# Optimization experiments

Measured on AMD Instinct MI355X. Metric: run time of the kernel, lower is better.

Reference implementation:

```python
import jax, jax.numpy as jnp
import numpy as np

BN_EPS = 1e-5
TAU = 1.0  # gumbel temperature

def setup_inputs() -> dict:
    key = jax.random.key(0)
    ks = jax.random.split(key, 6)
    B, O, F, H, HID = 32, 4096, 256, 8, 128
    x = jax.random.normal(ks[0], (B, O, F), dtype=jnp.float32)
    gumbel_noise = jax.random.gumbel(ks[1], (B, O, H), dtype=jnp.float32)
    W_in = jax.random.normal(ks[2], (F, HID), dtype=jnp.float32) * (1.0 / np.sqrt(F))
    b_in = jnp.zeros((HID,), jnp.float32)
    W_blk = jax.random.normal(ks[3], (HID, HID), dtype=jnp.float32) * (1.0 / np.sqrt(HID))
    b_blk = jnp.zeros((HID,), jnp.float32)
    bn_gamma = jnp.ones((HID,), jnp.float32)
    bn_beta = jnp.zeros((HID,), jnp.float32)
    W_fc = jax.random.normal(ks[4], (HID, H), dtype=jnp.float32) * (1.0 / np.sqrt(HID))
    b_fc = jnp.zeros((H,), jnp.float32)
    return {"x": x, "gumbel_noise": gumbel_noise, "W_in": W_in, "b_in": b_in,
            "W_blk": W_blk, "b_blk": b_blk, "bn_gamma": bn_gamma, "bn_beta": bn_beta,
            "W_fc": W_fc, "b_fc": b_fc}

def reference(x, gumbel_noise, W_in, b_in, W_blk, b_blk, bn_gamma, bn_beta, W_fc, b_fc):
    B, O, F = x.shape
    xf = x.reshape(B * O, F)
    # DynamicNetwork head: input linear + relu, one residual block (Linear+BN+ReLU), fc
    h = jax.nn.relu(xf @ W_in + b_in)  # (B*O, HID)
    z = h @ W_blk + b_blk
    mu = z.mean(axis=0)
    var = z.var(axis=0)  # biased var, matches BatchNorm training normalization
    z = (z - mu) * jax.lax.rsqrt(var + BN_EPS) * bn_gamma + bn_beta
    h = jax.nn.relu(z) + h  # residual
    logits = (h @ W_fc + b_fc).reshape(B, O, -1)  # (B, O, H)
    # mask out zero-norm observations
    mask = (jnp.linalg.norm(x, axis=2) != 0)[..., None].astype(x.dtype)  # (B, O, 1)
    logits = logits * mask
    # gumbel softmax over observation dim (soft)
    w = jax.nn.softmax((logits + gumbel_noise) / TAU, axis=1)  # (B, O, H)
    # weighted sum pooling: algebraically the repeat-multiply-sum in the original
    pooled = jnp.einsum('boh,bof->bhf', w, x)  # (B, H, F)
    return pooled.reshape(B, -1)  # (B, H*F)
```

## Files before the change

kernel.cpp:

```cpp
#include <hip/hip_runtime.h>
#include <hip/hip_bf16.h>
#include <math.h>

#define MB_ 131072
#define F_  256
#define HID_ 128
#define H_  8
#define O_  4096
#define B_  32

typedef __attribute__((ext_vector_type(8))) short short8;
typedef __attribute__((ext_vector_type(4))) float f32x4;

static __device__ __forceinline__ unsigned short f2bf(float f) {
    unsigned int u = __float_as_uint(f);
    unsigned int r = (u + 0x7fffu + ((u >> 16) & 1u)) >> 16;
    return (unsigned short)r;
}
static __device__ __forceinline__ float bf2f(unsigned short u) {
    return __uint_as_float(((unsigned int)u) << 16);
}

__global__ __launch_bounds__(256) void k_prep(
    const float* __restrict__ W_in, const float* __restrict__ W_blk,
    unsigned short* __restrict__ WinT, unsigned short* __restrict__ WblkT)
{
    const int idx = blockIdx.x * 256 + threadIdx.x;
    if (idx < 32768) {
        const int n = idx >> 8, k = idx & 255;
        WinT[idx] = f2bf(W_in[(size_t)k * HID_ + n]);
    } else {
        const int i2 = idx - 32768;
        const int n = i2 >> 7, k = i2 & 127;
        WblkT[i2] = f2bf(W_blk[(size_t)k * HID_ + n]);
    }
}

__global__ __launch_bounds__(256) void k_phaseA(
    const float* __restrict__ x, const unsigned short* __restrict__ WinT,
    const unsigned short* __restrict__ WblkT,
    const float* __restrict__ b_in, const float* __restrict__ b_blk,
    unsigned short* __restrict__ h_out, float* __restrict__ mask_out,
    float* __restrict__ sumP, float* __restrict__ sumsqP)
{
    __shared__ unsigned short a_s[128 * 40];
    __shared__ unsigned short b_s[128 * 40];
    __shared__ unsigned short hb_s[128 * 136];
    __shared__ float msum_s[128];
    __shared__ float csum_s[128], csumsq_s[128];

    const int tid = threadIdx.x;
    const int R0 = blockIdx.x * 128;
    const int lp_r = tid >> 3;
    const int lp_c = tid & 7;
    const int wave = tid >> 6;
    const int wrow = wave >> 1, wcol = wave & 1;
    const int lane = tid & 63;
    const int lm = lane & 15, quad = lane >> 4;

    if (tid < 128) { msum_s[tid] = 0.f; csum_s[tid] = 0.f; csumsq_s[tid] = 0.f; }
    float ms[4] = {0.f, 0.f, 0.f, 0.f};

    f32x4 acc[4][4];
#pragma unroll
    for (int i = 0; i < 4; i++)
#pragma unroll
        for (int j = 0; j < 4; j++) acc[i][j] = (f32x4){0.f, 0.f, 0.f, 0.f};

    for (int kt = 0; kt < 8; kt++) {
#pragma unroll
        for (int p = 0; p < 4; p++) {
            const int r = lp_r + 32 * p;
            const float4 v = *(const float4*)(x + (size_t)(R0 + r) * F_ + kt * 32 + lp_c * 4);
            ms[p] += v.x * v.x + v.y * v.y + v.z * v.z + v.w * v.w;
            ushort4 o;
            o.x = f2bf(v.x); o.y = f2bf(v.y); o.z = f2bf(v.z); o.w = f2bf(v.w);
            *(ushort4*)(&a_s[r * 40 + lp_c * 4]) = o;
        }
#pragma unroll
        for (int p = 0; p < 4; p++) {
            const int n = lp_r + 32 * p;
            const ushort4 wv = *(const ushort4*)(WinT + (size_t)n * F_ + kt * 32 + lp_c * 4);
            *(ushort4*)(&b_s[n * 40 + lp_c * 4]) = wv;
        }
        __syncthreads();
        short8 af[4], bfr[4];
#pragma unroll
        for (int mi = 0; mi < 4; mi++)
            af[mi] = *(const short8*)(&a_s[(wrow * 64 + mi * 16 + lm) * 40 + quad * 8]);
#pragma unroll
        for (int ni = 0; ni < 4; ni++)
            bfr[ni] = *(const short8*)(&b_s[(wcol * 64 + ni * 16 + lm) * 40 + quad * 8]);
#pragma unroll
        for (int mi = 0; mi < 4; mi++)
#pragma unroll
            for (int ni = 0; ni < 4; ni++)
                acc[mi][ni] = __builtin_amdgcn_mfma_f32_16x16x32_bf16(af[mi], bfr[ni], acc[mi][ni], 0, 0, 0);
        __syncthreads();
    }

#pragma unroll
    for (int p = 0; p < 4; p++) atomicAdd(&msum_s[lp_r + 32 * p], ms[p]);
    {
        float bcol[4];
#pragma unroll
        for (int ni = 0; ni < 4; ni++) bcol[ni] = b_in[wcol * 64 + ni * 16 + lm];
#pragma unroll
        for (int mi = 0; mi < 4; mi++)
#pragma unroll
            for (int r = 0; r < 4; r++) {
                const int row = wrow * 64 + mi * 16 + quad * 4 + r;
#pragma unroll
                for (int ni = 0; ni < 4; ni++) {
                    const int col = wcol * 64 + ni * 16 + lm;
                    hb_s[row * 136 + col] = f2bf(fmaxf(acc[mi][ni][r] + bcol[ni], 0.f));
                }
            }
    }
    __syncthreads();

    {
        const int row = tid >> 1, half = tid & 1;
#pragma unroll
        for (int c8 = 0; c8 < 8; c8++) {
            const short8 v = *(const short8*)(&hb_s[row * 136 + half * 64 + c8 * 8]);
            *(short8*)(h_out + (size_t)(R0 + row) * HID_ + half * 64 + c8 * 8) = v;
        }
    }
    if (tid < 128) mask_out[R0 + tid] = (msum_s[tid] != 0.f) ? 1.f : 0.f;

#pragma unroll
    for (int i = 0; i < 4; i++)
#pragma unroll
        for (int j = 0; j < 4; j++) acc[i][j] = (f32x4){0.f, 0.f, 0.f, 0.f};
    for (int kt = 0; kt < 4; kt++) {
#pragma unroll
        for (int p = 0; p < 4; p++) {
            const int n = lp_r + 32 * p;
            const ushort4 wv = *(const ushort4*)(WblkT + (size_t)n * HID_ + kt * 32 + lp_c * 4);
            *(ushort4*)(&b_s[n * 40 + lp_c * 4]) = wv;
        }
        __syncthreads();
        short8 af[4], bfr[4];
#pragma unroll
        for (int mi = 0; mi < 4; mi++)
            af[mi] = *(const short8*)(&hb_s[(wrow * 64 + mi * 16 + lm) * 136 + kt * 32 + quad * 8]);
#pragma unroll
        for (int ni = 0; ni < 4; ni++)
            bfr[ni] = *(const short8*)(&b_s[(wcol * 64 + ni * 16 + lm) * 40 + quad * 8]);
#pragma unroll
        for (int mi = 0; mi < 4; mi++)
#pragma unroll
            for (int ni = 0; ni < 4; ni++)
                acc[mi][ni] = __builtin_amdgcn_mfma_f32_16x16x32_bf16(af[mi], bfr[ni], acc[mi][ni], 0, 0, 0);
        __syncthreads();
    }

    {
        float bcol[4];
#pragma unroll
        for (int ni = 0; ni < 4; ni++) bcol[ni] = b_blk[wcol * 64 + ni * 16 + lm];
        float s_c[4] = {0.f, 0.f, 0.f, 0.f}, ss_c[4] = {0.f, 0.f, 0.f, 0.f};
#pragma unroll
        for (int mi = 0; mi < 4; mi++)
#pragma unroll
            for (int r = 0; r < 4; r++)
#pragma unroll
                for (int ni = 0; ni < 4; ni++) {
                    const float zv = acc[mi][ni][r] + bcol[ni];
                    s_c[ni] += zv;
                    ss_c[ni] += zv * zv;
                }
#pragma unroll
        for (int ni = 0; ni < 4; ni++) {
            atomicAdd(&csum_s[wcol * 64 + ni * 16 + lm], s_c[ni]);
            atomicAdd(&csumsq_s[wcol * 64 + ni * 16 + lm], ss_c[ni]);
        }
    }
    __syncthreads();
    if (tid < 128) {
        sumP[(size_t)blockIdx.x * 128 + tid] = csum_s[tid];
        sumsqP[(size_t)blockIdx.x * 128 + tid] = csumsq_s[tid];
    }
}

__global__ __launch_bounds__(256) void k_bnfin(
    const float* __restrict__ sumP, const float* __restrict__ sumsqP,
    const float* __restrict__ gamma, const float* __restrict__ beta,
    float* __restrict__ scale, float* __restrict__ shift)
{
    const int c = blockIdx.x;
    const int tid = threadIdx.x;
    float s = 0.f, ss = 0.f;
    for (int i = tid; i < 1024; i += 256) {
        s  += sumP[(size_t)i * 128 + c];
        ss += sumsqP[(size_t)i * 128 + c];
    }
#pragma unroll
    for (int off = 32; off; off >>= 1) {
        s  += __shfl_xor(s, off, 64);
        ss += __shfl_xor(ss, off, 64);
    }
    __shared__ float rs[4], rss[4];
    const int wid = tid >> 6, lane = tid & 63;
    if (lane == 0) { rs[wid] = s; rss[wid] = ss; }
    __syncthreads();
    if (tid == 0) {
        const float S  = rs[0] + rs[1] + rs[2] + rs[3];
        const float SS = rss[0] + rss[1] + rss[2] + rss[3];
        const float inv_m = 1.0f / (float)MB_;
        const float mu = S * inv_m;
        const float var = SS * inv_m - mu * mu;
        const float sc = gamma[c] * rsqrtf(var + 1e-5f);
        scale[c] = sc;
        shift[c] = beta[c] - mu * sc;
    }
}

__global__ __launch_bounds__(256) void k_phaseC(
    const unsigned short* __restrict__ h_in, const unsigned short* __restrict__ WblkT,
    const float* __restrict__ b_blk,
    const float* __restrict__ scale, const float* __restrict__ shift,
    const float* __restrict__ W_fc, const float* __restrict__ b_fc,
    const float* __restrict__ mask, const float* __restrict__ gumbel,
    float* __restrict__ t_bho)
{
    __shared__ unsigned short hb_s[128 * 136];
    __shared__ unsigned short b_s[128 * 40];
    __shared__ float wfc_s[128 * 8];
    __shared__ float sc_s[128], sh_s[128];

    const int tid = threadIdx.x;
    const int R0 = blockIdx.x * 128;
    const int wave = tid >> 6;
    const int wrow = wave >> 1, wcol = wave & 1;
    const int lane = tid & 63;
    const int lm = lane & 15, quad = lane >> 4;
    const int lp_r = tid >> 3, lp_c = tid & 7;

    for (int i = tid; i < 1024; i += 256) wfc_s[i] = W_fc[i];
    if (tid < 128) { sc_s[tid] = scale[tid]; sh_s[tid] = shift[tid]; }
    {
        const int row = tid >> 1, half = tid & 1;
#pragma unroll
        for (int c8 = 0; c8 < 8; c8++) {
            const short8 v = *(const short8*)(h_in + (size_t)(R0 + row) * HID_ + half * 64 + c8 * 8);
            *(short8*)(&hb_s[row * 136 + half * 64 + c8 * 8]) = v;
        }
    }
    __syncthreads();

    f32x4 acc[4][4];
#pragma unroll
    for (int i = 0; i < 4; i++)
#pragma unroll
        for (int j = 0; j < 4; j++) acc[i][j] = (f32x4){0.f, 0.f, 0.f, 0.f};
    for (int kt = 0; kt < 4; kt++) {
#pragma unroll
        for (int p = 0; p < 4; p++) {
            const int n = lp_r + 32 * p;
            const ushort4 wv = *(const ushort4*)(WblkT + (size_t)n * HID_ + kt * 32 + lp_c * 4);
            *(ushort4*)(&b_s[n * 40 + lp_c * 4]) = wv;
        }
        __syncthreads();
        short8 af[4], bfr[4];
#pragma unroll
        for (int mi = 0; mi < 4; mi++)
            af[mi] = *(const short8*)(&hb_s[(wrow * 64 + mi * 16 + lm) * 136 + kt * 32 + quad * 8]);
#pragma unroll
        for (int ni = 0; ni < 4; ni++)
            bfr[ni] = *(const short8*)(&b_s[(wcol * 64 + ni * 16 + lm) * 40 + quad * 8]);
#pragma unroll
        for (int mi = 0; mi < 4; mi++)
#pragma unroll
            for (int ni = 0; ni < 4; ni++)
                acc[mi][ni] = __builtin_amdgcn_mfma_f32_16x16x32_bf16(af[mi], bfr[ni], acc[mi][ni], 0, 0, 0);
        __syncthreads();
    }

    {
        float bcol[4];
#pragma unroll
        for (int ni = 0; ni < 4; ni++) bcol[ni] = b_blk[wcol * 64 + ni * 16 + lm];
#pragma unroll
        for (int mi = 0; mi < 4; mi++)
#pragma unroll
            for (int r = 0; r < 4; r++) {
                const int row = wrow * 64 + mi * 16 + quad * 4 + r;
#pragma unroll
                for (int ni = 0; ni < 4; ni++) {
                    const int col = wcol * 64 + ni * 16 + lm;
                    const float zv = acc[mi][ni][r] + bcol[ni];
                    const float hv = bf2f(hb_s[row * 136 + col]);
                    const float hb = fmaxf(zv * sc_s[col] + sh_s[col], 0.f) + hv;
                    hb_s[row * 136 + col] = f2bf(hb);
                }
            }
    }
    __syncthreads();

    if (tid < 128) {
        const int row = tid;
        const int grow = R0 + row;
        const int b = grow >> 12, o = grow & 4095;
        float a8[8];
#pragma unroll
        for (int j = 0; j < 8; j++) a8[j] = 0.f;
#pragma unroll 4
        for (int k8 = 0; k8 < 16; k8++) {
            const short8 hv8 = *(const short8*)(&hb_s[row * 136 + k8 * 8]);
#pragma unroll
            for (int e = 0; e < 8; e++) {
                const float hv = bf2f((unsigned short)hv8[e]);
                const int k = k8 * 8 + e;
#pragma unroll
                for (int j = 0; j < 8; j++) a8[j] += hv * wfc_s[k * 8 + j];
            }
        }
        const float mk = mask[grow];
        const float* gp = gumbel + (size_t)grow * 8;
#pragma unroll
        for (int j = 0; j < 8; j++) {
            const float t = (a8[j] + b_fc[j]) * mk + gp[j];
            t_bho[((size_t)(b * 8 + j)) * O_ + o] = t;
        }
    }
}

__global__ __launch_bounds__(256) void k_softmax(
    const float* __restrict__ t_in, float* __restrict__ w_out)
{
    const int bh = blockIdx.x;
    const int tid = threadIdx.x;
    const float* tp = t_in + (size_t)bh * O_;
    float4 v[4];
    float mx = -3.4e38f;
#pragma unroll
    for (int it = 0; it < 4; it++) {
        v[it] = *(const float4*)(tp + it * 1024 + tid * 4);
        mx = fmaxf(mx, fmaxf(fmaxf(v[it].x, v[it].y), fmaxf(v[it].z, v[it].w)));
    }
#pragma unroll
    for (int off = 32; off; off >>= 1) mx = fmaxf(mx, __shfl_xor(mx, off, 64));
    __shared__ float rm[4], rsum[4];
    const int wid = tid >> 6, lane = tid & 63;
    if (lane == 0) rm[wid] = mx;
    __syncthreads();
    mx = fmaxf(fmaxf(rm[0], rm[1]), fmaxf(rm[2], rm[3]));
    float sum = 0.f;
#pragma unroll
    for (int it = 0; it < 4; it++) {
        v[it].x = __expf(v[it].x - mx); v[it].y = __expf(v[it].y - mx);
        v[it].z = __expf(v[it].z - mx); v[it].w = __expf(v[it].w - mx);
        sum += v[it].x + v[it].y + v[it].z + v[it].w;
    }
#pragma unroll
    for (int off = 32; off; off >>= 1) sum += __shfl_xor(sum, off, 64);
    if (lane == 0) rsum[wid] = sum;
    __syncthreads();
    sum = rsum[0] + rsum[1] + rsum[2] + rsum[3];
    const float inv = 1.f / sum;
    float* wp = w_out + (size_t)bh * O_;
#pragma unroll
    for (int it = 0; it < 4; it++) {
        float4 o;
        o.x = v[it].x * inv; o.y = v[it].y * inv; o.z = v[it].z * inv; o.w = v[it].w * inv;
        *(float4*)(wp + it * 1024 + tid * 4) = o;
    }
}

__global__ __launch_bounds__(256) void k_pool(
    const float* __restrict__ x, const float* __restrict__ w_in,
    float* __restrict__ pp)
{
    __shared__ float ws_s[8][128];
    const int tid = threadIdx.x;
    const int oc = blockIdx.x;
    const int b = blockIdx.y;
    const int wave = tid >> 6, lane = tid & 63;
    const int f = wave * 64 + lane;
    for (int i = tid; i < 1024; i += 256) {
        const int hh = i >> 7, oi = i & 127;
        ws_s[hh][oi] = w_in[((size_t)(b * 8 + hh)) * O_ + oc * 128 + oi];
    }
    __syncthreads();
    float acc[8];
#pragma unroll
    for (int hh = 0; hh < 8; hh++) acc[hh] = 0.f;
    const float* xp = x + ((size_t)(b * O_ + oc * 128)) * F_ + f;
#pragma unroll 1
    for (int oi = 0; oi < 128; oi += 4) {
        float xv[4];
#pragma unroll
        for (int u = 0; u < 4; u++) xv[u] = xp[(size_t)(oi + u) * F_];
#pragma unroll
        for (int u = 0; u < 4; u++)
#pragma unroll
            for (int hh = 0; hh < 8; hh++) acc[hh] += ws_s[hh][oi + u] * xv[u];
    }
    float* outp = pp + ((size_t)(oc * 32 + b)) * 2048;
#pragma unroll
    for (int hh = 0; hh < 8; hh++) outp[hh * 256 + f] = acc[hh];
}

__global__ __launch_bounds__(256) void k_reduce_pool(
    const float* __restrict__ pp, float* __restrict__ out)
{
    const size_t i = (size_t)blockIdx.x * 256 + threadIdx.x;
    float s = 0.f;
#pragma unroll
    for (int oc = 0; oc < 32; oc++) s += pp[(size_t)oc * 65536 + i];
    out[i] = s;
}

extern "C" void kernel_launch(void* const* d_in, const int* in_sizes, int n_in,
                              void* d_out, int out_size, void* d_ws, size_t ws_size,
                              hipStream_t stream)
{
    const float* x      = (const float*)d_in[0];
    const float* gumbel = (const float*)d_in[1];
    const float* W_in   = (const float*)d_in[2];
    const float* b_in   = (const float*)d_in[3];
    const float* W_blk  = (const float*)d_in[4];
    const float* b_blk  = (const float*)d_in[5];
    const float* gamma  = (const float*)d_in[6];
    const float* beta   = (const float*)d_in[7];
    const float* W_fc   = (const float*)d_in[8];
    const float* b_fc   = (const float*)d_in[9];
    float* out = (float*)d_out;
    char* ws = (char*)d_ws;

    unsigned short* h_bf  = (unsigned short*)(ws + 0);
    float* mask   = (float*)(ws + 33554432);
    float* sumP   = (float*)(ws + 34078720);
    float* sumsqP = (float*)(ws + 34603008);
    float* scale  = (float*)(ws + 35127296);
    float* shift  = (float*)(ws + 35127808);
    float* t_buf  = (float*)(ws + 35128320);
    float* w_buf  = (float*)(ws + 39322624);
    float* pp     = (float*)(ws + 43516928);
    unsigned short* WinT  = (unsigned short*)(ws + 51905536);
    unsigned short* WblkT = (unsigned short*)(ws + 51971072);

    k_prep<<<192, 256, 0, stream>>>(W_in, W_blk, WinT, WblkT);
    k_phaseA<<<1024, 256, 0, stream>>>(x, WinT, WblkT, b_in, b_blk, h_bf, mask, sumP, sumsqP);
    k_bnfin<<<128, 256, 0, stream>>>(sumP, sumsqP, gamma, beta, scale, shift);
    k_phaseC<<<1024, 256, 0, stream>>>(h_bf, WblkT, b_blk, scale, shift, W_fc, b_fc, mask, gumbel, t_buf);
    k_softmax<<<256, 256, 0, stream>>>(t_buf, w_buf);
    k_pool<<<dim3(32, 32), 256, 0, stream>>>(x, w_buf, pp);
    k_reduce_pool<<<256, 256, 0, stream>>>(pp, out);
}
```

Before: 318.4 us.

## Load MFMA fragments directly from global memory, bypassing LDS staging

Phase A and phase C GEMM loops now load x and weight fragments from global memory straight into MFMA operand registers, converting x to bf16 in registers. This drops the LDS staging buffers and the per-k-tile barriers. The x row norm for the mask and the BN column sums are now reduced with wave shuffles before fewer shared atomics, and launch bounds request 4 blocks per SM. The cost is that the weight matrices are read redundantly by each wave from global/L2. The x reads are also less coalesced (32-byte chunks per lane across rows), and the occupancy hint may force register spills.

```diff
diff --git a/kernel.cpp b/kernel.cpp
--- a/kernel.cpp
+++ b/kernel.cpp
@@ -19,6 +19,13 @@
 }
 static __device__ __forceinline__ float bf2f(unsigned short u) {
     return __uint_as_float(((unsigned int)u) << 16);
+}
+static __device__ __forceinline__ unsigned int pk2bf(float a, float b) {
+    float2 f2; f2.x = a; f2.y = b;
+    __hip_bfloat162 h = __float22bfloat162_rn(f2);
+    union { __hip_bfloat162 h2; unsigned int u; } cv;
+    cv.h2 = h;
+    return cv.u;
 }
 
 __global__ __launch_bounds__(256) void k_prep(
@@ -36,71 +43,71 @@
     }
 }
 
-__global__ __launch_bounds__(256) void k_phaseA(
+__global__ __launch_bounds__(256, 4) void k_phaseA(
     const float* __restrict__ x, const unsigned short* __restrict__ WinT,
     const unsigned short* __restrict__ WblkT,
     const float* __restrict__ b_in, const float* __restrict__ b_blk,
     unsigned short* __restrict__ h_out, float* __restrict__ mask_out,
     float* __restrict__ sumP, float* __restrict__ sumsqP)
 {
-    __shared__ unsigned short a_s[128 * 40];
-    __shared__ unsigned short b_s[128 * 40];
     __shared__ unsigned short hb_s[128 * 136];
-    __shared__ float msum_s[128];
     __shared__ float csum_s[128], csumsq_s[128];
 
     const int tid = threadIdx.x;
     const int R0 = blockIdx.x * 128;
-    const int lp_r = tid >> 3;
-    const int lp_c = tid & 7;
     const int wave = tid >> 6;
     const int wrow = wave >> 1, wcol = wave & 1;
     const int lane = tid & 63;
     const int lm = lane & 15, quad = lane >> 4;
 
-    if (tid < 128) { msum_s[tid] = 0.f; csum_s[tid] = 0.f; csumsq_s[tid] = 0.f; }
+    if (tid < 128) { csum_s[tid] = 0.f; csumsq_s[tid] = 0.f; }
+
+    f32x4 acc[4][4];
+#pragma unroll
+    for (int i = 0; i < 4; i++)
+#pragma unroll
+        for (int j = 0; j < 4; j++) acc[i][j] = (f32x4){0.f, 0.f, 0.f, 0.f};
     float ms[4] = {0.f, 0.f, 0.f, 0.f};
 
-    f32x4 acc[4][4];
-#pragma unroll
-    for (int i = 0; i < 4; i++)
-#pragma unroll
-        for (int j = 0; j < 4; j++) acc[i][j] = (f32x4){0.f, 0.f, 0.f, 0.f};
-
+    const float* xb = x + (size_t)(R0 + wrow * 64 + lm) * F_;
+    const unsigned short* wb = WinT + (size_t)(wcol * 64 + lm) * F_;
+
+#pragma unroll 2
     for (int kt = 0; kt < 8; kt++) {
-#pragma unroll
-        for (int p = 0; p < 4; p++) {
-            const int r = lp_r + 32 * p;
-            const float4 v = *(const float4*)(x + (size_t)(R0 + r) * F_ + kt * 32 + lp_c * 4);
-            ms[p] += v.x * v.x + v.y * v.y + v.z * v.z + v.w * v.w;
-            ushort4 o;
-            o.x = f2bf(v.x); o.y = f2bf(v.y); o.z = f2bf(v.z); o.w = f2bf(v.w);
-            *(ushort4*)(&a_s[r * 40 + lp_c * 4]) = o;
-        }
-#pragma unroll
-        for (int p = 0; p < 4; p++) {
-            const int n = lp_r + 32 * p;
-            const ushort4 wv = *(const ushort4*)(WinT + (size_t)n * F_ + kt * 32 + lp_c * 4);
-            *(ushort4*)(&b_s[n * 40 + lp_c * 4]) = wv;
-        }
-        __syncthreads();
+        const int kof = kt * 32 + quad * 8;
         short8 af[4], bfr[4];
 #pragma unroll
-        for (int mi = 0; mi < 4; mi++)
-            af[mi] = *(const short8*)(&a_s[(wrow * 64 + mi * 16 + lm) * 40 + quad * 8]);
+        for (int mi = 0; mi < 4; mi++) {
+            const float4 v0 = *(const float4*)(xb + (size_t)mi * 16 * F_ + kof);
+            const float4 v1 = *(const float4*)(xb + (size_t)mi * 16 * F_ + kof + 4);
+            ms[mi] += v0.x * v0.x + v0.y * v0.y + v0.z * v0.z + v0.w * v0.w
+                    + v1.x * v1.x + v1.y * v1.y + v1.z * v1.z + v1.w * v1.w;
+            union { short8 s8; unsigned int u[4]; } fr;
+            fr.u[0] = pk2bf(v0.x, v0.y);
+            fr.u[1] = pk2bf(v0.z, v0.w);
+            fr.u[2] = pk2bf(v1.x, v1.y);
+            fr.u[3] = pk2bf(v1.z, v1.w);
+            af[mi] = fr.s8;
+        }
 #pragma unroll
         for (int ni = 0; ni < 4; ni++)
-            bfr[ni] = *(const short8*)(&b_s[(wcol * 64 + ni * 16 + lm) * 40 + quad * 8]);
+            bfr[ni] = *(const short8*)(wb + (size_t)ni * 16 * F_ + kof);
 #pragma unroll
         for (int mi = 0; mi < 4; mi++)
 #pragma unroll
             for (int ni = 0; ni < 4; ni++)
                 acc[mi][ni] = __builtin_amdgcn_mfma_f32_16x16x32_bf16(af[mi], bfr[ni], acc[mi][ni], 0, 0, 0);
-        __syncthreads();
-    }
-
-#pragma unroll
-    for (int p = 0; p < 4; p++) atomicAdd(&msum_s[lp_r + 32 * p], ms[p]);
+    }
+
+#pragma unroll
+    for (int mi = 0; mi < 4; mi++) {
+        float s = ms[mi];
+        s += __shfl_xor(s, 16);
+        s += __shfl_xor(s, 32);
+        if (wcol == 0 && quad == 0)
+            mask_out[R0 + wrow * 64 + mi * 16 + lm] = (s != 0.f) ? 1.f : 0.f;
+    }
+
     {
         float bcol[4];
 #pragma unroll
@@ -127,33 +134,27 @@
             *(short8*)(h_out + (size_t)(R0 + row) * HID_ + half * 64 + c8 * 8) = v;
         }
     }
-    if (tid < 128) mask_out[R0 + tid] = (msum_s[tid] != 0.f) ? 1.f : 0.f;
 
 #pragma unroll
     for (int i = 0; i < 4; i++)
 #pragma unroll
         for (int j = 0; j < 4; j++) acc[i][j] = (f32x4){0.f, 0.f, 0.f, 0.f};
+    const unsigned short* wb2 = WblkT + (size_t)(wcol * 64 + lm) * HID_;
+#pragma unroll
     for (int kt = 0; kt < 4; kt++) {
-#pragma unroll
-        for (int p = 0; p < 4; p++) {
-            const int n = lp_r + 32 * p;
-            const ushort4 wv = *(const ushort4*)(WblkT + (size_t)n * HID_ + kt * 32 + lp_c * 4);
-            *(ushort4*)(&b_s[n * 40 + lp_c * 4]) = wv;
-        }
-        __syncthreads();
+        const int kof = kt * 32 + quad * 8;
         short8 af[4], bfr[4];
 #pragma unroll
         for (int mi = 0; mi < 4; mi++)
-            af[mi] = *(const short8*)(&hb_s[(wrow * 64 + mi * 16 + lm) * 136 + kt * 32 + quad * 8]);
+            af[mi] = *(const short8*)(&hb_s[(wrow * 64 + mi * 16 + lm) * 136 + kof]);
 #pragma unroll
         for (int ni = 0; ni < 4; ni++)
-            bfr[ni] = *(const short8*)(&b_s[(wcol * 64 + ni * 16 + lm) * 40 + quad * 8]);
+            bfr[ni] = *(const short8*)(wb2 + (size_t)ni * 16 * HID_ + kof);
 #pragma unroll
         for (int mi = 0; mi < 4; mi++)
 #pragma unroll
             for (int ni = 0; ni < 4; ni++)
                 acc[mi][ni] = __builtin_amdgcn_mfma_f32_16x16x32_bf16(af[mi], bfr[ni], acc[mi][ni], 0, 0, 0);
-        __syncthreads();
     }
 
     {
@@ -173,8 +174,13 @@
                 }
 #pragma unroll
         for (int ni = 0; ni < 4; ni++) {
-            atomicAdd(&csum_s[wcol * 64 + ni * 16 + lm], s_c[ni]);
-            atomicAdd(&csumsq_s[wcol * 64 + ni * 16 + lm], ss_c[ni]);
+            float s = s_c[ni], ss = ss_c[ni];
+            s  += __shfl_xor(s, 16);  s  += __shfl_xor(s, 32);
+            ss += __shfl_xor(ss, 16); ss += __shfl_xor(ss, 32);
+            if (quad == 0) {
+                atomicAdd(&csum_s[wcol * 64 + ni * 16 + lm], s);
+                atomicAdd(&csumsq_s[wcol * 64 + ni * 16 + lm], ss);
+            }
         }
     }
     __syncthreads();
@@ -217,7 +223,7 @@
     }
 }
 
-__global__ __launch_bounds__(256) void k_phaseC(
+__global__ __launch_bounds__(256, 4) void k_phaseC(
     const unsigned short* __restrict__ h_in, const unsigned short* __restrict__ WblkT,
     const float* __restrict__ b_blk,
     const float* __restrict__ scale, const float* __restrict__ shift,
@@ -226,7 +232,6 @@
     float* __restrict__ t_bho)
 {
     __shared__ unsigned short hb_s[128 * 136];
-    __shared__ unsigned short b_s[128 * 40];
     __shared__ float wfc_s[128 * 8];
     __shared__ float sc_s[128], sh_s[128];
 
@@ -236,7 +241,6 @@
     const int wrow = wave >> 1, wcol = wave & 1;
     const int lane = tid & 63;
     const int lm = lane & 15, quad = lane >> 4;
-    const int lp_r = tid >> 3, lp_c = tid & 7;
 
     for (int i = tid; i < 1024; i += 256) wfc_s[i] = W_fc[i];
     if (tid < 128) { sc_s[tid] = scale[tid]; sh_s[tid] = shift[tid]; }
@@ -255,27 +259,22 @@
     for (int i = 0; i < 4; i++)
 #pragma unroll
         for (int j = 0; j < 4; j++) acc[i][j] = (f32x4){0.f, 0.f, 0.f, 0.f};
+    const unsigned short* wb2 = WblkT + (size_t)(wcol * 64 + lm) * HID_;
+#pragma unroll
     for (int kt = 0; kt < 4; kt++) {
-#pragma unroll
-        for (int p = 0; p < 4; p++) {
-            const int n = lp_r + 32 * p;
-            const ushort4 wv = *(const ushort4*)(WblkT + (size_t)n * HID_ + kt * 32 + lp_c * 4);
-            *(ushort4*)(&b_s[n * 40 + lp_c * 4]) = wv;
-        }
-        __syncthreads();
+        const int kof = kt * 32 + quad * 8;
         short8 af[4], bfr[4];
 #pragma unroll
         for (int mi = 0; mi < 4; mi++)
-            af[mi] = *(const short8*)(&hb_s[(wrow * 64 + mi * 16 + lm) * 136 + kt * 32 + quad * 8]);
+            af[mi] = *(const short8*)(&hb_s[(wrow * 64 + mi * 16 + lm) * 136 + kof]);
 #pragma unroll
         for (int ni = 0; ni < 4; ni++)
-            bfr[ni] = *(const short8*)(&b_s[(wcol * 64 + ni * 16 + lm) * 40 + quad * 8]);
+            bfr[ni] = *(const short8*)(wb2 + (size_t)ni * 16 * HID_ + kof);
 #pragma unroll
         for (int mi = 0; mi < 4; mi++)
 #pragma unroll
             for (int ni = 0; ni < 4; ni++)
                 acc[mi][ni] = __builtin_amdgcn_mfma_f32_16x16x32_bf16(af[mi], bfr[ni], acc[mi][ni], 0, 0, 0);
-        __syncthreads();
     }
 
     {
```

Measured after the change: 313.0 us. Within noise of the previous version (-1.7%).
